# Performance work log

Measured on AMD Instinct MI355X. Metric: run time of the kernel, lower is better.

The kernel has to match this reference:

```python
import jax, jax.numpy as jnp
import numpy as np

N, D, F, O = 32768, 32, 128, 128  # nodes, fixed in-degree, in_feats, out_feats


def _lstm_reduce(m, W_ih, W_hh, b_ih, b_hh):
    """Run an LSTM over each node's neighbor mailbox m: [N, T, F] -> final h: [N, H].
    PyTorch gate order: i, f, g, o. W_ih: [4H, F], W_hh: [4H, H]."""
    n, _, _ = m.shape
    H = W_hh.shape[1]
    b = b_ih + b_hh

    def step(carry, x_t):
        h, c = carry
        gates = x_t @ W_ih.T + h @ W_hh.T + b  # [N, 4H]
        i, f, g, o = jnp.split(gates, 4, axis=-1)
        c = jax.nn.sigmoid(f) * c + jax.nn.sigmoid(i) * jnp.tanh(g)
        h = jax.nn.sigmoid(o) * jnp.tanh(c)
        return (h, c), None

    h0 = jnp.zeros((n, H), m.dtype)
    (h_final, _), _ = jax.lax.scan(step, (h0, h0), jnp.swapaxes(m, 0, 1))
    return h_final


def setup_inputs() -> dict:
    key = jax.random.key(0)
    ks = jax.random.split(key, 9)
    stdv_lin = 1.0 / np.sqrt(F)   # linear init: uniform(-1/sqrt(in_feats))
    stdv_lstm = 1.0 / np.sqrt(F)  # torch LSTM init: uniform(-1/sqrt(hidden))
    u = lambda k, shape, s: jax.random.uniform(k, shape, jnp.float32, -s, s)
    return {
        "feat": jax.random.normal(ks[0], (N, F), jnp.float32),
        "neigh_idx": jax.random.randint(ks[1], (N, D), 0, N, jnp.int32),
        "W_ih": u(ks[2], (4 * F, F), stdv_lstm),
        "W_hh": u(ks[3], (4 * F, F), stdv_lstm),
        "b_ih": u(ks[4], (4 * F,), stdv_lstm),
        "b_hh": u(ks[5], (4 * F,), stdv_lstm),
        "W1": u(ks[6], (O, F), stdv_lin),
        "b1": u(ks[6], (O,), stdv_lin),
        "W2": u(ks[7], (O, F), stdv_lin),
        "b2": u(ks[8], (O,), stdv_lin),
    }


def reference(feat, neigh_idx, W_ih, W_hh, b_ih, b_hh, W1, b1, W2, b2):
    # Mailbox gather: each node's D neighbor feature rows -> [N, D, F]
    m = feat[neigh_idx]
    # LSTM reducer -> final hidden state per node
    h = _lstm_reduce(m, W_ih, W_hh, b_ih, b_hh)  # [N, F]
    degs = jnp.asarray(neigh_idx.shape[1], feat.dtype)  # fixed-degree graph
    ah = h / degs
    # feat = linear1(feat) + linear2(ah)
    return feat @ W1.T + b1 + ah @ W2.T + b2
```

## Files before the change

### kernel.cpp

```cpp
#include <hip/hip_runtime.h>
#include <hip/hip_bf16.h>

#define NN 32768
#define DEG 32
#define FF 128
#define OO 128
#define MB 32

#define K1 1.4426950408889634f
#define K2 2.8853900817779268f

#define PPITCH 1056
#define P0OFF 0
#define P1OFF 33792
#define H0OFF 67584
#define H1OFF 75776

typedef __attribute__((ext_vector_type(8))) short bfrag;
typedef __attribute__((ext_vector_type(4))) float f32x4;

__device__ __forceinline__ unsigned short b16(float x) {
    unsigned u = __float_as_uint(x) + 0x8000u;
    return (unsigned short)(u >> 16);
}
__device__ __forceinline__ float bf2f(unsigned short u) {
    return __uint_as_float((unsigned)u << 16);
}
__device__ __forceinline__ bfrag pack8(float4 a, float4 b) {
    bfrag r;
    r[0] = (short)b16(a.x); r[1] = (short)b16(a.y); r[2] = (short)b16(a.z); r[3] = (short)b16(a.w);
    r[4] = (short)b16(b.x); r[5] = (short)b16(b.y); r[6] = (short)b16(b.z); r[7] = (short)b16(b.w);
    return r;
}
__device__ __forceinline__ void gload16(const void* g, void* l) {
    __builtin_amdgcn_global_load_lds(
        (const __attribute__((address_space(1))) unsigned int*)g,
        (__attribute__((address_space(3))) unsigned int*)l, 16, 0, 0);
}

__global__ void prep_weights(const float* __restrict__ wih, const float* __restrict__ whh,
                             const float* __restrict__ b_ih, const float* __restrict__ b_hh,
                             const float* __restrict__ w1, const float* __restrict__ b1,
                             const float* __restrict__ w2, const float* __restrict__ b2,
                             short* __restrict__ wihb, short* __restrict__ whhb,
                             short* __restrict__ w1b, short* __restrict__ w2b,
                             float* __restrict__ biasg, float* __restrict__ biaso)
{
    int i = blockIdx.x * blockDim.x + threadIdx.x;
    if (i < 512 * 128) { wihb[i] = (short)b16(wih[i]); whhb[i] = (short)b16(whh[i]); }
    if (i < 128 * 128) { w1b[i] = (short)b16(w1[i]); w2b[i] = (short)b16(w2[i] * 0.03125f); }
    if (i < 512) biasg[i] = b_ih[i] + b_hh[i];
    if (i < 128) biaso[i] = b1[i] + b2[i];
}

__global__ __launch_bounds__(512, 2)
void xp_gemm(const float* __restrict__ feat, const short* __restrict__ wihb,
             const float* __restrict__ biasg, unsigned short* __restrict__ xp)
{
    __shared__ short xt[MB * 128];

    const int tid  = (int)threadIdx.x;
    const int lane = tid & 63;
    const int wave = tid >> 6;
    const int n0   = (int)blockIdx.x * MB;
    const int srow = tid >> 4;
    const int cs   = tid & 15;

    {   const float4* p = reinterpret_cast<const float4*>(feat + (n0 + srow) * FF + cs * 8);
        int sb = (srow * 256 + cs * 16) ^ ((srow & 7) << 4);
        *reinterpret_cast<bfrag*>(reinterpret_cast<char*>(xt) + sb) = pack8(p[0], p[1]); }

    const int colw = wave * 16 + (lane & 15);
    bfrag wih[4][4];
#pragma unroll
    for (int g = 0; g < 4; ++g) {
        const short* pih = wihb + (g * 128 + colw) * FF + (lane >> 4) * 8;
#pragma unroll
        for (int kt = 0; kt < 4; ++kt)
            wih[g][kt] = *reinterpret_cast<const bfrag*>(pih + kt * 32);
    }
    float bg4[4];
#pragma unroll
    for (int g = 0; g < 4; ++g) bg4[g] = biasg[g * 128 + colw];

    __syncthreads();

    const int arow = lane & 15;
    const int asub = (lane >> 4) * 16;
    const int hr0  = (lane >> 4) * 4;
    const int swz  = (arow & 7) << 4;
    const char* xtp = reinterpret_cast<const char*>(xt);

#pragma unroll
    for (int rt = 0; rt < 2; ++rt) {
        bfrag a[4];
#pragma unroll
        for (int kt = 0; kt < 4; ++kt)
            a[kt] = *reinterpret_cast<const bfrag*>(xtp + (((rt * 16 + arow) * 256 + kt * 64 + asub) ^ swz));
#pragma unroll
        for (int g = 0; g < 4; ++g) {
            f32x4 acc = {bg4[g], bg4[g], bg4[g], bg4[g]};
#pragma unroll
            for (int kt = 0; kt < 4; ++kt)
                acc = __builtin_amdgcn_mfma_f32_16x16x32_bf16(a[kt], wih[g][kt], acc, 0, 0, 0);
#pragma unroll
            for (int r = 0; r < 4; ++r)
                xp[(n0 + rt * 16 + hr0 + r) * 512 + g * 128 + colw] = b16(acc[r]);
        }
    }
}

__global__ __launch_bounds__(512, 2)
void sage_xp(const float* __restrict__ feat, const int* __restrict__ nidx,
             const unsigned short* __restrict__ xp,
             const short* __restrict__ whhb, const short* __restrict__ w1b,
             const short* __restrict__ w2b, const float* __restrict__ biaso,
             float* __restrict__ out)
{
    __shared__ char lds[83968];
    __shared__ int  idx_s[MB * DEG];

    const int tid  = (int)threadIdx.x;
    const int lane = tid & 63;
    const int wave = tid >> 6;
    const int n0   = (int)blockIdx.x * MB;
    const int srow = tid >> 4;
    const int cs   = tid & 15;

    idx_s[tid]       = nidx[n0 * DEG + tid];
    idx_s[512 + tid] = nidx[n0 * DEG + 512 + tid];
    {   bfrag z = {0, 0, 0, 0, 0, 0, 0, 0};
        *reinterpret_cast<bfrag*>(lds + H0OFF + tid * 16) = z; }

    const int colw = wave * 16 + (lane & 15);
    bfrag whh[4][4];
#pragma unroll
    for (int g = 0; g < 4; ++g) {
        const short* phh = whhb + (g * 128 + colw) * FF + (lane >> 4) * 8;
#pragma unroll
        for (int kt = 0; kt < 4; ++kt)
            whh[g][kt] = *reinterpret_cast<const bfrag*>(phh + kt * 32);
    }
    __syncthreads();

#pragma unroll
    for (int j = 0; j < 4; ++j) {
        int nd = idx_s[(wave * 4 + j) * DEG + 0];
        gload16(xp + nd * 512 + lane * 8, lds + P0OFF + (wave * 4 + j) * PPITCH);
    }
    __syncthreads();

    const int arow = lane & 15;
    const int asub = (lane >> 4) * 16;
    const int hr0  = (lane >> 4) * 4;
    const int swz  = (arow & 7) << 4;

    f32x4 cs0 = {0.f, 0.f, 0.f, 0.f};
    f32x4 cs1 = {0.f, 0.f, 0.f, 0.f};

    auto rdP = [&](const char* pc, int goff) {
        f32x4 v;
        v[0] = bf2f(*reinterpret_cast<const unsigned short*>(pc + goff));
        v[1] = bf2f(*reinterpret_cast<const unsigned short*>(pc + goff + PPITCH));
        v[2] = bf2f(*reinterpret_cast<const unsigned short*>(pc + goff + 2 * PPITCH));
        v[3] = bf2f(*reinterpret_cast<const unsigned short*>(pc + goff + 3 * PPITCH));
        return v;
    };

    auto dort = [&](int rt, int pcur, int hcur, int hnxt, f32x4& cst) {
        bfrag ha[4];
#pragma unroll
        for (int kt = 0; kt < 4; ++kt)
            ha[kt] = *reinterpret_cast<const bfrag*>(
                lds + hcur + (((rt * 16 + arow) * 256 + kt * 64 + asub) ^ swz));
        const char* pc = lds + pcur + (rt * 16 + hr0) * PPITCH + colw * 2;
        f32x4 gi = rdP(pc, 0), gf = rdP(pc, 256), gg = rdP(pc, 512), go = rdP(pc, 768);
#pragma unroll
        for (int kt = 0; kt < 4; ++kt) {
            gi = __builtin_amdgcn_mfma_f32_16x16x32_bf16(ha[kt], whh[0][kt], gi, 0, 0, 0);
            gf = __builtin_amdgcn_mfma_f32_16x16x32_bf16(ha[kt], whh[1][kt], gf, 0, 0, 0);
            gg = __builtin_amdgcn_mfma_f32_16x16x32_bf16(ha[kt], whh[2][kt], gg, 0, 0, 0);
            go = __builtin_amdgcn_mfma_f32_16x16x32_bf16(ha[kt], whh[3][kt], go, 0, 0, 0);
        }
#pragma unroll
        for (int r = 0; r < 4; ++r) {
            float av = __builtin_amdgcn_exp2f(-K1 * gi[r]);
            float bv = __builtin_amdgcn_exp2f(K2 * fminf(gg[r], 40.0f));
            float dv = __builtin_amdgcn_exp2f(-K1 * gf[r]);
            float ev = __builtin_amdgcn_exp2f(-K1 * go[r]);
            float t1 = __builtin_amdgcn_rcpf((1.0f + av) * (1.0f + bv));
            float t2 = __builtin_amdgcn_rcpf(1.0f + dv);
            float c  = fmaf(cst[r], t2, (bv - 1.0f) * t1);
            cst[r] = c;
            float uv = __builtin_amdgcn_exp2f(K2 * c);
            float t3 = __builtin_amdgcn_rcpf((1.0f + ev) * (1.0f + uv));
            float h  = (uv - 1.0f) * t3;
            int hrow = rt * 16 + hr0 + r;
            int hb   = (hrow * 256 + colw * 2) ^ ((hrow & 7) << 4);
            *reinterpret_cast<unsigned short*>(lds + hnxt + hb) = b16(h);
        }
    };

#define STEP(T, PCUR, PNXT, HCUR, HNXT)                                         \
    {                                                                           \
        if ((T) < DEG - 1) {                                                    \
            _Pragma("unroll")                                                   \
            for (int j = 0; j < 4; ++j) {                                       \
                int nd = idx_s[(wave * 4 + j) * DEG + (T) + 1];                 \
                gload16(xp + nd * 512 + lane * 8,                               \
                        lds + (PNXT) + (wave * 4 + j) * PPITCH);                \
            }                                                                   \
        }                                                                       \
        dort(0, PCUR, HCUR, HNXT, cs0);                                         \
        dort(1, PCUR, HCUR, HNXT, cs1);                                         \
        __syncthreads();                                                        \
    }

#pragma unroll 1
    for (int tt = 0; tt < DEG; tt += 2) {
        STEP(tt,     P0OFF, P1OFF, H0OFF, H1OFF);
        STEP(tt + 1, P1OFF, P0OFF, H1OFF, H0OFF);
    }
#undef STEP

    {   const float4* p = reinterpret_cast<const float4*>(feat + (n0 + srow) * FF + cs * 8);
        int sb = (srow * 256 + cs * 16) ^ ((srow & 7) << 4);
        *reinterpret_cast<bfrag*>(lds + P0OFF + sb) = pack8(p[0], p[1]); }
    __syncthreads();

    bfrag w1f[4], w2f[4];
#pragma unroll
    for (int kt = 0; kt < 4; ++kt) {
        w1f[kt] = *reinterpret_cast<const bfrag*>(w1b + colw * FF + kt * 32 + (lane >> 4) * 8);
        w2f[kt] = *reinterpret_cast<const bfrag*>(w2b + colw * FF + kt * 32 + (lane >> 4) * 8);
    }
    const float bb = biaso[colw];
#pragma unroll
    for (int rt = 0; rt < 2; ++rt) {
        bfrag fa[4], hfa[4];
#pragma unroll
        for (int kt = 0; kt < 4; ++kt) {
            int byte = ((rt * 16 + arow) * 256 + kt * 64 + asub) ^ swz;
            fa[kt]  = *reinterpret_cast<const bfrag*>(lds + P0OFF + byte);
            hfa[kt] = *reinterpret_cast<const bfrag*>(lds + H0OFF + byte);
        }
        f32x4 acc = {0.f, 0.f, 0.f, 0.f};
#pragma unroll
        for (int kt = 0; kt < 4; ++kt) {
            acc = __builtin_amdgcn_mfma_f32_16x16x32_bf16(fa[kt],  w1f[kt], acc, 0, 0, 0);
            acc = __builtin_amdgcn_mfma_f32_16x16x32_bf16(hfa[kt], w2f[kt], acc, 0, 0, 0);
        }
#pragma unroll
        for (int r = 0; r < 4; ++r) {
            int orow = n0 + rt * 16 + hr0 + r;
            out[orow * OO + colw] = acc[r] + bb;
        }
    }
}

__global__ __launch_bounds__(512, 2)
void sage_lstm_fb(const float* __restrict__ featf, const int* __restrict__ nidx,
                  const short* __restrict__ wihb, const short* __restrict__ whhb,
                  const short* __restrict__ w1b, const short* __restrict__ w2b,
                  const float* __restrict__ biasg, const float* __restrict__ biaso,
                  float* __restrict__ out)
{
    __shared__ short xbuf[2][MB * 128];
    __shared__ short hbuf[2][MB * 128];
    __shared__ int   idx_s[MB * DEG];

    const int tid  = (int)threadIdx.x;
    const int lane = tid & 63;
    const int wave = tid >> 6;
    const int n0   = (int)blockIdx.x * MB;
    const int srow = tid >> 4;
    const int cs   = tid & 15;

    idx_s[tid]       = nidx[n0 * DEG + tid];
    idx_s[512 + tid] = nidx[n0 * DEG + 512 + tid];
    {   bfrag z = {0, 0, 0, 0, 0, 0, 0, 0};
        reinterpret_cast<bfrag*>(hbuf[0])[tid] = z; }

    const int colw = wave * 16 + (lane & 15);
    bfrag wih[4][4], whh[4][4];
#pragma unroll
    for (int g = 0; g < 4; ++g) {
        const short* pih = wihb + (g * 128 + colw) * FF + (lane >> 4) * 8;
        const short* phh = whhb + (g * 128 + colw) * FF + (lane >> 4) * 8;
#pragma unroll
        for (int kt = 0; kt < 4; ++kt) {
            wih[g][kt] = *reinterpret_cast<const bfrag*>(pih + kt * 32);
            whh[g][kt] = *reinterpret_cast<const bfrag*>(phh + kt * 32);
        }
    }
    const float bi = biasg[colw];
    const float bf = biasg[128 + colw];
    const float bg = biasg[256 + colw];
    const float bo = biasg[384 + colw];
    const f32x4 bvi = {bi, bi, bi, bi};
    const f32x4 bvf = {bf, bf, bf, bf};
    const f32x4 bvg = {bg, bg, bg, bg};
    const f32x4 bvo = {bo, bo, bo, bo};

    __syncthreads();
    {
        const float4* p = reinterpret_cast<const float4*>(featf + idx_s[srow * DEG] * FF + cs * 8);
        int sb = (srow * 256 + cs * 16) ^ ((srow & 7) << 4);
        *reinterpret_cast<bfrag*>(reinterpret_cast<char*>(xbuf[0]) + sb) = pack8(p[0], p[1]);
    }
    __syncthreads();

    const int arow = lane & 15;
    const int asub = (lane >> 4) * 16;
    const int hr0  = (lane >> 4) * 4;
    const int swz  = (arow & 7) << 4;

    auto mm4 = [&](const char* p, int rbase, const bfrag (&W)[4][4],
                   f32x4& vi, f32x4& vf, f32x4& vg, f32x4& vo) {
        bfrag a[4];
#pragma unroll
        for (int kt = 0; kt < 4; ++kt)
            a[kt] = *reinterpret_cast<const bfrag*>(p + ((rbase * 256 + kt * 64 + asub) ^ swz));
#pragma unroll
        for (int kt = 0; kt < 4; ++kt) {
            vi = __builtin_amdgcn_mfma_f32_16x16x32_bf16(a[kt], W[0][kt], vi, 0, 0, 0);
            vf = __builtin_amdgcn_mfma_f32_16x16x32_bf16(a[kt], W[1][kt], vf, 0, 0, 0);
            vg = __builtin_amdgcn_mfma_f32_16x16x32_bf16(a[kt], W[2][kt], vg, 0, 0, 0);
            vo = __builtin_amdgcn_mfma_f32_16x16x32_bf16(a[kt], W[3][kt], vo, 0, 0, 0);
        }
    };
    auto actw = [&](f32x4& gi, f32x4& gf, f32x4& gg, f32x4& go,
                    f32x4& cst, char* hnxt, int rt) {
#pragma unroll
        for (int r = 0; r < 4; ++r) {
            float av = __builtin_amdgcn_exp2f(-K1 * gi[r]);
            float bv = __builtin_amdgcn_exp2f(K2 * fminf(gg[r], 40.0f));
            float dv = __builtin_amdgcn_exp2f(-K1 * gf[r]);
            float ev = __builtin_amdgcn_exp2f(-K1 * go[r]);
            float t1 = __builtin_amdgcn_rcpf((1.0f + av) * (1.0f + bv));
            float t2 = __builtin_amdgcn_rcpf(1.0f + dv);
            float c  = fmaf(cst[r], t2, (bv - 1.0f) * t1);
            cst[r] = c;
            float uv = __builtin_amdgcn_exp2f(K2 * c);
            float t3 = __builtin_amdgcn_rcpf((1.0f + ev) * (1.0f + uv));
            float h  = (uv - 1.0f) * t3;
            int hrow = rt * 16 + hr0 + r;
            int hb   = (hrow * 256 + colw * 2) ^ ((hrow & 7) << 4);
            *reinterpret_cast<unsigned short*>(hnxt + hb) = b16(h);
        }
    };

    f32x4 p0i, p0f, p0g, p0o, p1i, p1f, p1g, p1o;
    {
        char* x0p = reinterpret_cast<char*>(xbuf[0]);
        p0i = bvi; p0f = bvf; p0g = bvg; p0o = bvo;
        mm4(x0p, arow, wih, p0i, p0f, p0g, p0o);
        p1i = bvi; p1f = bvf; p1g = bvg; p1o = bvo;
        mm4(x0p, 16 + arow, wih, p1i, p1f, p1g, p1o);
    }
    {
        const float4* p = reinterpret_cast<const float4*>(featf + idx_s[srow * DEG + 1] * FF + cs * 8);
        int sb = (srow * 256 + cs * 16) ^ ((srow & 7) << 4);
        *reinterpret_cast<bfrag*>(reinterpret_cast<char*>(xbuf[1]) + sb) = pack8(p[0], p[1]);
    }
    __syncthreads();

    const f32x4 zz = {0.f, 0.f, 0.f, 0.f};
    f32x4 cs0 = zz, cs1 = zz;

#pragma unroll 2
    for (int t = 0; t < DEG; ++t) {
        const int cur = t & 1;
        char* hcur = reinterpret_cast<char*>(hbuf[cur]);
        char* hnxt = reinterpret_cast<char*>(hbuf[cur ^ 1]);
        char* xrd  = reinterpret_cast<char*>(xbuf[cur ^ 1]);
        char* xwr  = reinterpret_cast<char*>(xbuf[cur]);

        bfrag pre2;
        if (t < DEG - 2) {
            const float4* p = reinterpret_cast<const float4*>(featf + idx_s[srow * DEG + t + 2] * FF + cs * 8);
            pre2 = pack8(p[0], p[1]);
        }
        {
            f32x4 gi = p0i, gf = p0f, gg = p0g, go = p0o;
            mm4(hcur, arow, whh, gi, gf, gg, go);
            if (t < DEG - 1) {
                p0i = bvi; p0f = bvf; p0g = bvg; p0o = bvo;
                mm4(xrd, arow, wih, p0i, p0f, p0g, p0o);
            }
            actw(gi, gf, gg, go, cs0, hnxt, 0);
        }
        {
            f32x4 gi = p1i, gf = p1f, gg = p1g, go = p1o;
            mm4(hcur, 16 + arow, whh, gi, gf, gg, go);
            if (t < DEG - 1) {
                p1i = bvi; p1f = bvf; p1g = bvg; p1o = bvo;
                mm4(xrd, 16 + arow, wih, p1i, p1f, p1g, p1o);
            }
            actw(gi, gf, gg, go, cs1, hnxt, 1);
        }
        if (t < DEG - 2) {
            int sb = (srow * 256 + cs * 16) ^ ((srow & 7) << 4);
            *reinterpret_cast<bfrag*>(xwr + sb) = pre2;
        }
        __syncthreads();
    }

    {
        const float4* p = reinterpret_cast<const float4*>(featf + (n0 + srow) * FF + cs * 8);
        int sb = (srow * 256 + cs * 16) ^ ((srow & 7) << 4);
        *reinterpret_cast<bfrag*>(reinterpret_cast<char*>(xbuf[0]) + sb) = pack8(p[0], p[1]);
    }
    __syncthreads();

    char* const x0p = reinterpret_cast<char*>(xbuf[0]);
    char* const h0p = reinterpret_cast<char*>(hbuf[0]);
    bfrag w1f[4], w2f[4];
#pragma unroll
    for (int kt = 0; kt < 4; ++kt) {
        w1f[kt] = *reinterpret_cast<const bfrag*>(w1b + colw * FF + kt * 32 + (lane >> 4) * 8);
        w2f[kt] = *reinterpret_cast<const bfrag*>(w2b + colw * FF + kt * 32 + (lane >> 4) * 8);
    }
    const float bb = biaso[colw];
#pragma unroll
    for (int rt = 0; rt < 2; ++rt) {
        bfrag fa[4], hfa[4];
#pragma unroll
        for (int kt = 0; kt < 4; ++kt) {
            int byte = ((rt * 16 + arow) * 256 + kt * 64 + asub) ^ swz;
            fa[kt]  = *reinterpret_cast<const bfrag*>(x0p + byte);
            hfa[kt] = *reinterpret_cast<const bfrag*>(h0p + byte);
        }
        f32x4 acc = {0.f, 0.f, 0.f, 0.f};
#pragma unroll
        for (int kt = 0; kt < 4; ++kt) {
            acc = __builtin_amdgcn_mfma_f32_16x16x32_bf16(fa[kt],  w1f[kt], acc, 0, 0, 0);
            acc = __builtin_amdgcn_mfma_f32_16x16x32_bf16(hfa[kt], w2f[kt], acc, 0, 0, 0);
        }
#pragma unroll
        for (int r = 0; r < 4; ++r) {
            int orow = n0 + rt * 16 + hr0 + r;
            out[orow * OO + colw] = acc[r] + bb;
        }
    }
}

extern "C" void kernel_launch(void* const* d_in, const int* in_sizes, int n_in,
                              void* d_out, int out_size, void* d_ws, size_t ws_size,
                              hipStream_t stream)
{
    const float* feat = (const float*)d_in[0];
    const int*   nidx = (const int*)d_in[1];
    const float* W_ih = (const float*)d_in[2];
    const float* W_hh = (const float*)d_in[3];
    const float* b_ih = (const float*)d_in[4];
    const float* b_hh = (const float*)d_in[5];
    const float* W1   = (const float*)d_in[6];
    const float* b1   = (const float*)d_in[7];
    const float* W2   = (const float*)d_in[8];
    const float* b2   = (const float*)d_in[9];
    float* out = (float*)d_out;

    char* ws = (char*)d_ws;
    short* wihb  = (short*)(ws);
    short* whhb  = (short*)(ws + 131072);
    short* w1b   = (short*)(ws + 262144);
    short* w2b   = (short*)(ws + 294912);
    float* biasg = (float*)(ws + 327680);
    float* biaso = (float*)(ws + 329728);
    unsigned short* xpb = (unsigned short*)(ws + 330240);

    const size_t need = 330240 + (size_t)NN * 512 * 2;

    prep_weights<<<256, 256, 0, stream>>>(W_ih, W_hh, b_ih, b_hh, W1, b1, W2, b2,
                                          wihb, whhb, w1b, w2b, biasg, biaso);
    if (ws_size >= need) {
        xp_gemm<<<NN / MB, 512, 0, stream>>>(feat, wihb, biasg, xpb);
        sage_xp<<<NN / MB, 512, 0, stream>>>(feat, nidx, xpb, whhb, w1b, w2b, biaso, out);
    } else {
        sage_lstm_fb<<<NN / MB, 512, 0, stream>>>(feat, nidx, wihb, whhb,
                                                  w1b, w2b, biasg, biaso, out);
    }
}
```

Measured before the change: 359.4 us.

## Halve recurrent block to 16 nodes with 4 waves each owning two column tiles

The recurrent LSTM kernel now processes 16 nodes per block with 256 threads (4 waves) instead of 32 nodes with 512 threads. Each wave covers two 16-column tiles and holds twice the W_hh fragments in registers, reusing one h A-fragment load across both tiles. LDS usage roughly halves, so more blocks can be resident and more independent recurrences run per CU to hide the serial step latency and the gather loads. The cost is higher register pressure from the doubled weight fragments, which risks spills or lower occupancy. The gather loop still indexes idx_s by wave*4+j, which at 4 waves covers exactly 16 rows, so it stays consistent.

```diff
diff --git a/kernel.cpp b/kernel.cpp
--- a/kernel.cpp
+++ b/kernel.cpp
@@ -6,15 +6,17 @@
 #define FF 128
 #define OO 128
 #define MB 32
+#define MB2 16
 
 #define K1 1.4426950408889634f
 #define K2 2.8853900817779268f
 
-#define PPITCH 1056
+#define PPITCH 1040
 #define P0OFF 0
-#define P1OFF 33792
-#define H0OFF 67584
-#define H1OFF 75776
+#define P1OFF 16640
+#define H0OFF 33280
+#define H1OFF 37376
+#define LDSSZ 41472
 
 typedef __attribute__((ext_vector_type(8))) short bfrag;
 typedef __attribute__((ext_vector_type(4))) float f32x4;
@@ -110,37 +112,39 @@
     }
 }
 
-__global__ __launch_bounds__(512, 2)
-void sage_xp(const float* __restrict__ feat, const int* __restrict__ nidx,
-             const unsigned short* __restrict__ xp,
-             const short* __restrict__ whhb, const short* __restrict__ w1b,
-             const short* __restrict__ w2b, const float* __restrict__ biaso,
-             float* __restrict__ out)
+__global__ __launch_bounds__(256, 2)
+void sage_xp2(const float* __restrict__ feat, const int* __restrict__ nidx,
+              const unsigned short* __restrict__ xp,
+              const short* __restrict__ whhb, const short* __restrict__ w1b,
+              const short* __restrict__ w2b, const float* __restrict__ biaso,
+              float* __restrict__ out)
 {
-    __shared__ char lds[83968];
-    __shared__ int  idx_s[MB * DEG];
+    __shared__ char lds[LDSSZ];
+    __shared__ int  idx_s[MB2 * DEG];
 
     const int tid  = (int)threadIdx.x;
     const int lane = tid & 63;
     const int wave = tid >> 6;
-    const int n0   = (int)blockIdx.x * MB;
+    const int n0   = (int)blockIdx.x * MB2;
     const int srow = tid >> 4;
     const int cs   = tid & 15;
 
     idx_s[tid]       = nidx[n0 * DEG + tid];
-    idx_s[512 + tid] = nidx[n0 * DEG + 512 + tid];
+    idx_s[256 + tid] = nidx[n0 * DEG + 256 + tid];
     {   bfrag z = {0, 0, 0, 0, 0, 0, 0, 0};
         *reinterpret_cast<bfrag*>(lds + H0OFF + tid * 16) = z; }
 
-    const int colw = wave * 16 + (lane & 15);
-    bfrag whh[4][4];
-#pragma unroll
-    for (int g = 0; g < 4; ++g) {
-        const short* phh = whhb + (g * 128 + colw) * FF + (lane >> 4) * 8;
-#pragma unroll
-        for (int kt = 0; kt < 4; ++kt)
-            whh[g][kt] = *reinterpret_cast<const bfrag*>(phh + kt * 32);
-    }
+    const int colb = wave * 32 + (lane & 15);
+    bfrag whh[2][4][4];
+#pragma unroll
+    for (int ct = 0; ct < 2; ++ct)
+#pragma unroll
+        for (int g = 0; g < 4; ++g) {
+            const short* phh = whhb + (g * 128 + colb + ct * 16) * FF + (lane >> 4) * 8;
+#pragma unroll
+            for (int kt = 0; kt < 4; ++kt)
+                whh[ct][g][kt] = *reinterpret_cast<const bfrag*>(phh + kt * 32);
+        }
     __syncthreads();
 
 #pragma unroll
@@ -167,20 +171,16 @@
         return v;
     };
 
-    auto dort = [&](int rt, int pcur, int hcur, int hnxt, f32x4& cst) {
-        bfrag ha[4];
-#pragma unroll
-        for (int kt = 0; kt < 4; ++kt)
-            ha[kt] = *reinterpret_cast<const bfrag*>(
-                lds + hcur + (((rt * 16 + arow) * 256 + kt * 64 + asub) ^ swz));
-        const char* pc = lds + pcur + (rt * 16 + hr0) * PPITCH + colw * 2;
+    auto doct = [&](int ct, const bfrag (&ha)[4], int pcur, int hnxt, f32x4& cst) {
+        const int colw = colb + ct * 16;
+        const char* pc = lds + pcur + hr0 * PPITCH + colw * 2;
         f32x4 gi = rdP(pc, 0), gf = rdP(pc, 256), gg = rdP(pc, 512), go = rdP(pc, 768);
 #pragma unroll
         for (int kt = 0; kt < 4; ++kt) {
-            gi = __builtin_amdgcn_mfma_f32_16x16x32_bf16(ha[kt], whh[0][kt], gi, 0, 0, 0);
-            gf = __builtin_amdgcn_mfma_f32_16x16x32_bf16(ha[kt], whh[1][kt], gf, 0, 0, 0);
-            gg = __builtin_amdgcn_mfma_f32_16x16x32_bf16(ha[kt], whh[2][kt], gg, 0, 0, 0);
-            go = __builtin_amdgcn_mfma_f32_16x16x32_bf16(ha[kt], whh[3][kt], go, 0, 0, 0);
+            gi = __builtin_amdgcn_mfma_f32_16x16x32_bf16(ha[kt], whh[ct][0][kt], gi, 0, 0, 0);
+            gf = __builtin_amdgcn_mfma_f32_16x16x32_bf16(ha[kt], whh[ct][1][kt], gf, 0, 0, 0);
+            gg = __builtin_amdgcn_mfma_f32_16x16x32_bf16(ha[kt], whh[ct][2][kt], gg, 0, 0, 0);
+            go = __builtin_amdgcn_mfma_f32_16x16x32_bf16(ha[kt], whh[ct][3][kt], go, 0, 0, 0);
         }
 #pragma unroll
         for (int r = 0; r < 4; ++r) {
@@ -195,7 +195,7 @@
             float uv = __builtin_amdgcn_exp2f(K2 * c);
             float t3 = __builtin_amdgcn_rcpf((1.0f + ev) * (1.0f + uv));
             float h  = (uv - 1.0f) * t3;
-            int hrow = rt * 16 + hr0 + r;
+            int hrow = hr0 + r;
             int hb   = (hrow * 256 + colw * 2) ^ ((hrow & 7) << 4);
             *reinterpret_cast<unsigned short*>(lds + hnxt + hb) = b16(h);
         }
@@ -211,8 +211,13 @@
                         lds + (PNXT) + (wave * 4 + j) * PPITCH);                \
             }                                                                   \
         }                                                                       \
-        dort(0, PCUR, HCUR, HNXT, cs0);                                         \
-        dort(1, PCUR, HCUR, HNXT, cs1);                                         \
+        bfrag ha[4];                                                            \
+        _Pragma("unroll")                                                       \
+        for (int kt = 0; kt < 4; ++kt)                                          \
+            ha[kt] = *reinterpret_cast<const bfrag*>(                           \
+                lds + (HCUR) + ((arow * 256 + kt * 64 + asub) ^ swz));          \
+        doct(0, ha, PCUR, HNXT, cs0);                                           \
+        doct(1, ha, PCUR, HNXT, cs1);                                           \
         __syncthreads();                                                        \
     }
 
@@ -228,32 +233,37 @@
         *reinterpret_cast<bfrag*>(lds + P0OFF + sb) = pack8(p[0], p[1]); }
     __syncthreads();
 
-    bfrag w1f[4], w2f[4];
+    bfrag w1f[2][4], w2f[2][4];
+    float bb[2];
+#pragma unroll
+    for (int ct = 0; ct < 2; ++ct) {
+        const int colw = colb + ct * 16;
+#pragma unroll
+        for (int kt = 0; kt < 4; ++kt) {
+            w1f[ct][kt] = *reinterpret_cast<const bfrag*>(w1b + colw * FF + kt * 32 + (lane >> 4) * 8);
+            w2f[ct][kt] = *reinterpret_cast<const bfrag*>(w2b + colw * FF + kt * 32 + (lane >> 4) * 8);
+        }
+        bb[ct] = biaso[colw];
+    }
+    bfrag fa[4], hfa[4];
 #pragma unroll
     for (int kt = 0; kt < 4; ++kt) {
-        w1f[kt] = *reinterpret_cast<const bfrag*>(w1b + colw * FF + kt * 32 + (lane >> 4) * 8);
-        w2f[kt] = *reinterpret_cast<const bfrag*>(w2b + colw * FF + kt * 32 + (lane >> 4) * 8);
-    }
-    const float bb = biaso[colw];
-#pragma unroll
-    for (int rt = 0; rt < 2; ++rt) {
-        bfrag fa[4], hfa[4];
-#pragma unroll
-        for (int kt = 0; kt < 4; ++kt) {
-            int byte = ((rt * 16 + arow) * 256 + kt * 64 + asub) ^ swz;
-            fa[kt]  = *reinterpret_cast<const bfrag*>(lds + P0OFF + byte);
-            hfa[kt] = *reinterpret_cast<const bfrag*>(lds + H0OFF + byte);
-        }
+        int byte = (arow * 256 + kt * 64 + asub) ^ swz;
+        fa[kt]  = *reinterpret_cast<const bfrag*>(lds + P0OFF + byte);
+        hfa[kt] = *reinterpret_cast<const bfrag*>(lds + H0OFF + byte);
+    }
+#pragma unroll
+    for (int ct = 0; ct < 2; ++ct) {
         f32x4 acc = {0.f, 0.f, 0.f, 0.f};
 #pragma unroll
         for (int kt = 0; kt < 4; ++kt) {
-            acc = __builtin_amdgcn_mfma_f32_16x16x32_bf16(fa[kt],  w1f[kt], acc, 0, 0, 0);
-            acc = __builtin_amdgcn_mfma_f32_16x16x32_bf16(hfa[kt], w2f[kt], acc, 0, 0, 0);
+            acc = __builtin_amdgcn_mfma_f32_16x16x32_bf16(fa[kt],  w1f[ct][kt], acc, 0, 0, 0);
+            acc = __builtin_amdgcn_mfma_f32_16x16x32_bf16(hfa[kt], w2f[ct][kt], acc, 0, 0, 0);
         }
 #pragma unroll
         for (int r = 0; r < 4; ++r) {
-            int orow = n0 + rt * 16 + hr0 + r;
-            out[orow * OO + colw] = acc[r] + bb;
+            int orow = n0 + hr0 + r;
+            out[orow * OO + colb + ct * 16] = acc[r] + bb[ct];
         }
     }
 }
@@ -476,7 +486,7 @@
                                           wihb, whhb, w1b, w2b, biasg, biaso);
     if (ws_size >= need) {
         xp_gemm<<<NN / MB, 512, 0, stream>>>(feat, wihb, biasg, xpb);
-        sage_xp<<<NN / MB, 512, 0, stream>>>(feat, nidx, xpb, whhb, w1b, w2b, biaso, out);
+        sage_xp2<<<NN / MB2, 256, 0, stream>>>(feat, nidx, xpb, whhb, w1b, w2b, biaso, out);
     } else {
         sage_lstm_fb<<<NN / MB, 512, 0, stream>>>(feat, nidx, wihb, whhb,
                                                   w1b, w2b, biasg, biaso, out);
```

New measurement: 307.5 us. 14.4% less time.
